# Performance work log

Measured on AMD Instinct MI355X. Metric: run time of the kernel, lower is better.

Reference implementation:

```python
import jax, jax.numpy as jnp
import numpy as np

N = 100000      # num graph nodes
E = 1600000     # num edges (avg degree 16)
IN = 128        # in_channels
H = 128         # hidden_channels
B = 4096        # query batch
CTX = 20        # context set length (indices[:, 3:])


def setup_inputs() -> dict:
    key = jax.random.key(0)
    ks = jax.random.split(key, 16)
    inp = {
        "indices": jax.random.randint(ks[0], (B, 3 + CTX), 0, N, dtype=jnp.int64),
        "src": jax.random.randint(ks[1], (E,), 0, N, dtype=jnp.int32),
        "dst": jax.random.randint(ks[2], (E,), 0, N, dtype=jnp.int32),
        "w": jax.random.uniform(ks[3], (E,), dtype=jnp.float32),
        # learned params
        "ndata": jax.random.normal(ks[4], (N, IN), dtype=jnp.float32),
        "W1": jax.random.normal(ks[5], (H, IN), dtype=jnp.float32) * (1.0 / np.sqrt(IN)),
        "b1": jnp.zeros((H,), jnp.float32),
        "W2": jax.random.normal(ks[6], (H, H), dtype=jnp.float32) * (1.0 / np.sqrt(H)),
        "b2": jnp.zeros((H,), jnp.float32),
        "eps": jnp.zeros((2,), jnp.float32),  # learn_eps, one per GINConv
        "Wc1": jax.random.normal(ks[7], (H, 3 * H), dtype=jnp.float32) * (1.0 / np.sqrt(3 * H)),
        "bc1": jnp.zeros((H,), jnp.float32),
        "Wc2": jax.random.normal(ks[8], (H // 2, H), dtype=jnp.float32) * (1.0 / np.sqrt(H)),
        "bc2": jnp.zeros((H // 2,), jnp.float32),
        "Wc3": jax.random.normal(ks[9], (1, H // 2), dtype=jnp.float32) * (1.0 / np.sqrt(H // 2)),
        "bc3": jnp.zeros((1,), jnp.float32),
    }
    return inp


def _gin_conv(x, src, dst, w, deg, eps, W, b):
    # DGL GINConv(mean, learn_eps): h = lin((1+eps)*x + mean_{in-edges}(w_e * x_src))
    msg = w[:, None] * x[src]                                   # [E, D]
    agg = jax.ops.segment_sum(msg, dst, num_segments=N) / deg   # [N, D]
    return ((1.0 + eps) * x + agg) @ W.T + b


def reference(indices, src, dst, w, ndata, W1, b1, W2, b2, eps,
              Wc1, bc1, Wc2, bc2, Wc3, bc3):
    deg = jax.ops.segment_sum(jnp.ones((E,), ndata.dtype), dst, num_segments=N)
    deg = jnp.maximum(deg, 1.0)[:, None]

    x = ndata
    x = jax.nn.relu(_gin_conv(x, src, dst, w, deg, eps[0], W1, b1))  # dropout inactive (eval)
    x = _gin_conv(x, src, dst, w, deg, eps[1], W2, b2)               # last layer: no relu
    x = x.at[0].set(0.0)                                             # x[0] = zeros

    ing1 = x[indices[:, 0]]   # [B, H]
    ing2 = x[indices[:, 1]]   # [B, H]

    # embed_context: mean over nonzero-index context members
    ctx_idx = indices[:, 3:]                                   # [B, CTX]
    ctx_sum = x[ctx_idx].sum(axis=1)                           # [B, H]
    norm = jnp.maximum((ctx_idx > 0).sum(axis=1), 1).astype(x.dtype)[:, None]
    ctx = ctx_sum / norm

    y = jnp.concatenate([ing1, ing2, ctx], axis=1)             # [B, 3H]
    y = jax.nn.relu(y @ Wc1.T + bc1)
    y = jax.nn.relu(y @ Wc2.T + bc2)
    y = y @ Wc3.T + bc3                                        # [B, 1]
    return y
```

## Files before the change

### kernel.cpp

```cpp
#include <hip/hip_runtime.h>


#define CONV_NPB 32

__global__ void init_kernel(const float* __restrict__ W1, const float* __restrict__ W2,
                            const float* __restrict__ Wc1, const float* __restrict__ Wc2,
                            float* __restrict__ Wt1, float* __restrict__ Wt2,
                            float* __restrict__ Wc1t, float* __restrict__ Wc2t,
                            int* __restrict__ cnt, int n) {
  int i = blockIdx.x * blockDim.x + threadIdx.x;
  if (i < n) cnt[i] = 0;
  if (i < 16384) {
    int f = i >> 7, k = i & 127;
    Wt1[k * 128 + f] = W1[i];
  } else if (i < 32768) {
    int j = i - 16384; int f = j >> 7, k = j & 127;
    Wt2[k * 128 + f] = W2[j];
  } else if (i < 81920) {
    int j = i - 32768; int f = j / 384, k = j % 384;
    Wc1t[k * 128 + f] = Wc1[j];
  } else if (i < 90112) {
    int j = i - 81920; int f = j >> 7, k = j & 127;
    Wc2t[k * 64 + f] = Wc2[j];
  }
}

__global__ void hist_kernel(const int* __restrict__ dst, int* __restrict__ cnt,
                            int* __restrict__ rank, int E) {
  int e = blockIdx.x * blockDim.x + threadIdx.x;
  if (e < E) rank[e] = atomicAdd(&cnt[dst[e]], 1);
}

__global__ void scan1_kernel(const int* __restrict__ cnt, int* __restrict__ prow,
                             int* __restrict__ bsum, int n) {
  __shared__ int smem[256];
  const int t = threadIdx.x;
  const int base = blockIdx.x * 2048 + t * 8;
  int v[8];
  int s = 0;
#pragma unroll
  for (int j = 0; j < 8; ++j) {
    int idx = base + j;
    v[j] = (idx < n) ? ((cnt[idx] + 7) & ~7) : 0;
    s += v[j];
  }
  smem[t] = s;
  __syncthreads();
  for (int off = 1; off < 256; off <<= 1) {
    int add = (t >= off) ? smem[t - off] : 0;
    __syncthreads();
    smem[t] += add;
    __syncthreads();
  }
  int run = smem[t] - s;
  if (t == 255) bsum[blockIdx.x] = smem[255];
#pragma unroll
  for (int j = 0; j < 8; ++j) {
    int idx = base + j;
    if (idx < n) prow[idx] = run;
    run += v[j];
  }
}

__global__ void scan2_kernel(int* __restrict__ bsum, int nb) {
  const int t = threadIdx.x;
  if (nb <= 64) {
    const int orig = (t < nb) ? bsum[t] : 0;
    int v = orig;
#pragma unroll
    for (int off = 1; off < 64; off <<= 1) {
      int u = __shfl_up(v, off);
      if (t >= off) v += u;
    }
    if (t == nb - 1) bsum[nb] = v;
    if (t < nb) bsum[t] = v - orig;
  } else if (t == 0) {
    int run = 0;
    for (int i = 0; i < nb; ++i) { int v = bsum[i]; bsum[i] = run; run += v; }
    bsum[nb] = run;
  }
}

__global__ void scatter_kernel(const int* __restrict__ src, const int* __restrict__ dst,
                               const float* __restrict__ w, const int* __restrict__ prow,
                               const int* __restrict__ bsum,
                               const int* __restrict__ rank, int2* __restrict__ epack, int E) {
  int e = blockIdx.x * blockDim.x + threadIdx.x;
  if (e < E) {
    const int d = dst[e];
    const int pos = prow[d] + bsum[d >> 11] + rank[e];
    epack[pos] = make_int2(src[e], __float_as_int(w[e]));
  }
}

__launch_bounds__(256, 6)
__global__ void conv_kernel(const float* __restrict__ xin, float* __restrict__ xout,
                            const int* __restrict__ prow, const int* __restrict__ bsum,
                            const int* __restrict__ cnt,
                            const int2* __restrict__ epack,
                            const float* __restrict__ Wt,
                            const float* __restrict__ bias, const float* __restrict__ eps,
                            int epsidx, int dorelu, int zerorow0, int n, int nchunk) {
  __shared__ float xm[CONV_NPB * 128];
  __shared__ int rp_s[CONV_NPB + 1];
  const int t = threadIdx.x;
  const int nb = blockIdx.x * CONV_NPB;
  const float epsv = 1.0f + eps[epsidx];

#pragma unroll
  for (int i = 0; i < 4; ++i)
    *(float4*)&xm[(t + i * 256) * 4] = make_float4(0.f, 0.f, 0.f, 0.f);
  if (t <= CONV_NPB) {
    const int node = nb + t;
    rp_s[t] = (node >= n) ? bsum[nchunk] : (prow[node] + bsum[node >> 11]);
  }
  __syncthreads();

  {
    const int L = t >> 5;
    const int lane = t & 31;
    const int f0 = lane * 4;
    const int e0 = rp_s[0], eT = rp_s[CONV_NPB];
    const int nbat = (eT - e0) >> 3;
    const int chunk = (((nbat + 7) >> 3)) << 3;
    const int jb = e0 + L * chunk;
    const int je = min(jb + chunk, eT);
    if (jb < je) {
      const int4* ep4 = (const int4*)epack;
      int r = 0;
      while (rp_s[r + 1] <= jb) ++r;
      float4 acc = make_float4(0.f, 0.f, 0.f, 0.f);
      for (int j = jb; j < je; j += 8) {
        if (rp_s[r + 1] <= j) {
          float* bp = &xm[r * 128 + lane];
          atomicAdd(bp + 0,  acc.x);
          atomicAdd(bp + 32, acc.y);
          atomicAdd(bp + 64, acc.z);
          atomicAdd(bp + 96, acc.w);
          acc = make_float4(0.f, 0.f, 0.f, 0.f);
          do { ++r; } while (rp_s[r + 1] <= j);
        }
        const int h = j >> 1;
        const int4 q0 = ep4[h + 0];
        const int4 q1 = ep4[h + 1];
        const int4 q2 = ep4[h + 2];
        const int4 q3 = ep4[h + 3];
        const float4 a0 = *(const float4*)&xin[(size_t)q0.x * 128 + f0];
        const float4 a1 = *(const float4*)&xin[(size_t)q0.z * 128 + f0];
        const float4 a2 = *(const float4*)&xin[(size_t)q1.x * 128 + f0];
        const float4 a3 = *(const float4*)&xin[(size_t)q1.z * 128 + f0];
        const float4 a4 = *(const float4*)&xin[(size_t)q2.x * 128 + f0];
        const float4 a5 = *(const float4*)&xin[(size_t)q2.z * 128 + f0];
        const float4 a6 = *(const float4*)&xin[(size_t)q3.x * 128 + f0];
        const float4 a7 = *(const float4*)&xin[(size_t)q3.z * 128 + f0];
        const float w0 = __int_as_float(q0.y), w1 = __int_as_float(q0.w);
        const float w2 = __int_as_float(q1.y), w3 = __int_as_float(q1.w);
        const float w4 = __int_as_float(q2.y), w5 = __int_as_float(q2.w);
        const float w6 = __int_as_float(q3.y), w7 = __int_as_float(q3.w);
        acc.x += w0 * a0.x + w1 * a1.x + w2 * a2.x + w3 * a3.x
               + w4 * a4.x + w5 * a5.x + w6 * a6.x + w7 * a7.x;
        acc.y += w0 * a0.y + w1 * a1.y + w2 * a2.y + w3 * a3.y
               + w4 * a4.y + w5 * a5.y + w6 * a6.y + w7 * a7.y;
        acc.z += w0 * a0.z + w1 * a1.z + w2 * a2.z + w3 * a3.z
               + w4 * a4.z + w5 * a5.z + w6 * a6.z + w7 * a7.z;
        acc.w += w0 * a0.w + w1 * a1.w + w2 * a2.w + w3 * a3.w
               + w4 * a4.w + w5 * a5.w + w6 * a6.w + w7 * a7.w;
      }
      float* bp = &xm[r * 128 + lane];
      atomicAdd(bp + 0,  acc.x);
      atomicAdd(bp + 32, acc.y);
      atomicAdd(bp + 64, acc.z);
      atomicAdd(bp + 96, acc.w);
    }
  }
  __syncthreads();

  {
    float4 m[4];
#pragma unroll
    for (int q = 0; q < 4; ++q) {
      const int task = t + q * 256;
      const int r = task >> 5;
      const int fg = task & 31;
      m[q].x = xm[r * 128 + fg];
      m[q].y = xm[r * 128 + 32 + fg];
      m[q].z = xm[r * 128 + 64 + fg];
      m[q].w = xm[r * 128 + 96 + fg];
    }
    __syncthreads();
#pragma unroll
    for (int q = 0; q < 4; ++q) {
      const int task = t + q * 256;
      const int r = task >> 5;
      const int fg = task & 31;
      const int f0 = fg * 4;
      const int node = nb + r;
      float4 v = make_float4(0.f, 0.f, 0.f, 0.f);
      if (node < n) {
        const int d = cnt[node];
        const float rdeg = 1.0f / (float)(d > 1 ? d : 1);
        const float4 xv = *(const float4*)&xin[(size_t)node * 128 + f0];
        v.x = epsv * xv.x + m[q].x * rdeg;
        v.y = epsv * xv.y + m[q].y * rdeg;
        v.z = epsv * xv.z + m[q].z * rdeg;
        v.w = epsv * xv.w + m[q].w * rdeg;
      }
      *(float4*)&xm[r * 128 + f0] = v;
    }
  }
  __syncthreads();

  {
    const int fg = t & 31;
    const int rg = t >> 5;
    const int f0 = fg * 4;
    const int r0 = rg * 4;
    float4 acc[4];
#pragma unroll
    for (int r = 0; r < 4; ++r) acc[r] = make_float4(0.f, 0.f, 0.f, 0.f);
    for (int k = 0; k < 128; k += 4) {
      const float4 w0 = *(const float4*)&Wt[(k + 0) * 128 + f0];
      const float4 w1 = *(const float4*)&Wt[(k + 1) * 128 + f0];
      const float4 w2 = *(const float4*)&Wt[(k + 2) * 128 + f0];
      const float4 w3 = *(const float4*)&Wt[(k + 3) * 128 + f0];
#pragma unroll
      for (int r = 0; r < 4; ++r) {
        const float4 xv = *(const float4*)&xm[(r0 + r) * 128 + k];
        acc[r].x += xv.x * w0.x + xv.y * w1.x + xv.z * w2.x + xv.w * w3.x;
        acc[r].y += xv.x * w0.y + xv.y * w1.y + xv.z * w2.y + xv.w * w3.y;
        acc[r].z += xv.x * w0.z + xv.y * w1.z + xv.z * w2.z + xv.w * w3.z;
        acc[r].w += xv.x * w0.w + xv.y * w1.w + xv.z * w2.w + xv.w * w3.w;
      }
    }
    const float4 bv = *(const float4*)&bias[f0];
#pragma unroll
    for (int r = 0; r < 4; ++r) {
      const int node = nb + r0 + r;
      if (node < n) {
        float4 v;
        v.x = acc[r].x + bv.x;
        v.y = acc[r].y + bv.y;
        v.z = acc[r].z + bv.z;
        v.w = acc[r].w + bv.w;
        if (dorelu) {
          v.x = fmaxf(v.x, 0.f); v.y = fmaxf(v.y, 0.f);
          v.z = fmaxf(v.z, 0.f); v.w = fmaxf(v.w, 0.f);
        }
        if (zerorow0 && node == 0) { v.x = 0.f; v.y = 0.f; v.z = 0.f; v.w = 0.f; }
        *(float4*)&xout[(size_t)node * 128 + f0] = v;
      }
    }
  }
}

__launch_bounds__(256, 4)
__global__ void final_kernel(const float* __restrict__ x2, const int* __restrict__ indices,
                             const float* __restrict__ Wc1t, const float* __restrict__ bc1,
                             const float* __restrict__ Wc2t, const float* __restrict__ bc2,
                             const float* __restrict__ Wc3, const float* __restrict__ bc3,
                             float* __restrict__ out) {
  __shared__ float ysm[16 * 384];
  __shared__ float h1s[16 * 128];
  __shared__ float h2s[16 * 64];
  __shared__ float ccs[16];
  const int t = threadIdx.x;
  const int b0 = blockIdx.x * 16;

#pragma unroll
  for (int q = 0; q < 8; ++q) {
    const int s = t + q * 256;
    ysm[(s >> 7) * 384 + 256 + (s & 127)] = 0.f;
  }
  if (t < 16) {
    const int* ind = indices + (size_t)(b0 + t) * 23;
    int cc = 0;
#pragma unroll
    for (int j = 0; j < 20; ++j) cc += (ind[3 + j] > 0) ? 1 : 0;
    ccs[t] = 1.0f / (float)(cc > 0 ? cc : 1);
  }
  __syncthreads();

  {
    const int f = t & 127;
    const int half = t >> 7;
#pragma unroll 1
    for (int e = 0; e < 16; ++e) {
      const int* ind = indices + (size_t)(b0 + e) * 23;
      const int ing = ind[half];
      ysm[e * 384 + half * 128 + f] = x2[(size_t)ing * 128 + f];
      float cs = 0.f;
#pragma unroll
      for (int j = 0; j < 10; ++j) {
        const int cj = ind[3 + half * 10 + j];
        cs += x2[(size_t)cj * 128 + f];
      }
      atomicAdd(&ysm[e * 384 + 256 + f], cs);
    }
  }
  __syncthreads();
#pragma unroll
  for (int q = 0; q < 8; ++q) {
    const int s = t + q * 256;
    const int e = s >> 7;
    ysm[e * 384 + 256 + (s & 127)] *= ccs[e];
  }
  __syncthreads();

  {
    const int f1 = t & 127;
    const int eh = t >> 7;
    float acc[8];
    const float b = bc1[f1];
#pragma unroll
    for (int i = 0; i < 8; ++i) acc[i] = b;
    for (int k = 0; k < 384; k += 4) {
      const float wv0 = Wc1t[(k + 0) * 128 + f1];
      const float wv1 = Wc1t[(k + 1) * 128 + f1];
      const float wv2 = Wc1t[(k + 2) * 128 + f1];
      const float wv3 = Wc1t[(k + 3) * 128 + f1];
#pragma unroll
      for (int i = 0; i < 8; ++i) {
        const float4 yv = *(const float4*)&ysm[(eh * 8 + i) * 384 + k];
        acc[i] += yv.x * wv0 + yv.y * wv1 + yv.z * wv2 + yv.w * wv3;
      }
    }
#pragma unroll
    for (int i = 0; i < 8; ++i)
      h1s[(eh * 8 + i) * 128 + f1] = fmaxf(acc[i], 0.f);
  }
  __syncthreads();

  {
    const int f2 = t & 63;
    const int eg = t >> 6;
    float acc[4];
    const float b = bc2[f2];
#pragma unroll
    for (int i = 0; i < 4; ++i) acc[i] = b;
    for (int k = 0; k < 128; k += 4) {
      const float wv0 = Wc2t[(k + 0) * 64 + f2];
      const float wv1 = Wc2t[(k + 1) * 64 + f2];
      const float wv2 = Wc2t[(k + 2) * 64 + f2];
      const float wv3 = Wc2t[(k + 3) * 64 + f2];
#pragma unroll
      for (int i = 0; i < 4; ++i) {
        const float4 hv = *(const float4*)&h1s[(eg * 4 + i) * 128 + k];
        acc[i] += hv.x * wv0 + hv.y * wv1 + hv.z * wv2 + hv.w * wv3;
      }
    }
#pragma unroll
    for (int i = 0; i < 4; ++i)
      h2s[(eg * 4 + i) * 64 + f2] = fmaxf(acc[i], 0.f);
  }
  __syncthreads();

  {
    const int e = t >> 4;
    const int l = t & 15;
    float p = 0.f;
#pragma unroll
    for (int k = 0; k < 4; ++k)
      p += h2s[e * 64 + l + k * 16] * Wc3[l + k * 16];
#pragma unroll
    for (int o = 8; o > 0; o >>= 1) p += __shfl_down(p, o, 16);
    if (l == 0) out[b0 + e] = p + bc3[0];
  }
}

extern "C" void kernel_launch(void* const* d_in, const int* in_sizes, int n_in,
                              void* d_out, int out_size, void* d_ws, size_t ws_size,
                              hipStream_t stream) {
  const int* indices = (const int*)d_in[0];
  const int* src = (const int*)d_in[1];
  const int* dst = (const int*)d_in[2];
  const float* w = (const float*)d_in[3];
  const float* ndata = (const float*)d_in[4];
  const float* W1 = (const float*)d_in[5];
  const float* b1 = (const float*)d_in[6];
  const float* W2 = (const float*)d_in[7];
  const float* b2 = (const float*)d_in[8];
  const float* eps = (const float*)d_in[9];
  const float* Wc1 = (const float*)d_in[10];
  const float* bc1 = (const float*)d_in[11];
  const float* Wc2 = (const float*)d_in[12];
  const float* bc2 = (const float*)d_in[13];
  const float* Wc3 = (const float*)d_in[14];
  const float* bc3 = (const float*)d_in[15];
  float* out = (float*)d_out;

  const int E = in_sizes[1];
  const int N = in_sizes[4] / 128;
  const int B = in_sizes[0] / 23;

  char* ws = (char*)d_ws;
  size_t off = 0;
  auto alloc = [&](size_t bytes) -> char* {
    char* p = ws + off;
    off = (off + bytes + 255) & ~(size_t)255;
    return p;
  };
  const size_t Epad = (size_t)E + 8 * (size_t)N;
  int* cnt = (int*)alloc((size_t)N * 4);
  int* prow = (int*)alloc((size_t)(N + 1) * 4);
  int* rank = (int*)alloc((size_t)E * 4);
  int* bsum = (int*)alloc(256 * 4);
  int2* epack = (int2*)alloc(Epad * 8);
  float* x1 = (float*)alloc((size_t)N * 128 * 4);
  float* x2 = (float*)alloc((size_t)N * 128 * 4);
  float* Wt1 = (float*)alloc(16384 * 4);
  float* Wt2 = (float*)alloc(16384 * 4);
  float* Wc1t = (float*)alloc(49152 * 4);
  float* Wc2t = (float*)alloc(8192 * 4);

  hipMemsetAsync(epack, 0, Epad * 8, stream);

  const int ninit = (N > 90112) ? N : 90112;
  init_kernel<<<(ninit + 255) / 256, 256, 0, stream>>>(W1, W2, Wc1, Wc2, Wt1, Wt2, Wc1t, Wc2t, cnt, N);
  hist_kernel<<<(E + 255) / 256, 256, 0, stream>>>(dst, cnt, rank, E);
  const int nchunk = (N + 2047) / 2048;
  scan1_kernel<<<nchunk, 256, 0, stream>>>(cnt, prow, bsum, N);
  scan2_kernel<<<1, 64, 0, stream>>>(bsum, nchunk);
  scatter_kernel<<<(E + 255) / 256, 256, 0, stream>>>(src, dst, w, prow, bsum, rank, epack, E);

  const int nconv = (N + CONV_NPB - 1) / CONV_NPB;
  conv_kernel<<<nconv, 256, 0, stream>>>(ndata, x1, prow, bsum, cnt, epack, Wt1, b1, eps, 0, 1, 0, N, nchunk);
  conv_kernel<<<nconv, 256, 0, stream>>>(x1, x2, prow, bsum, cnt, epack, Wt2, b2, eps, 1, 0, 1, N, nchunk);

  final_kernel<<<B / 16, 256, 0, stream>>>(x2, indices, Wc1t, bc1, Wc2t, bc2, Wc3, bc3, out);
}
```

Before: 601.4 us.

## Vectorize edge preprocessing and restructure final MLP with fewer queries per block

The histogram and scatter kernels now handle two edges per thread with int2/float2 loads, cutting thread count and load instructions. The final kernel processes 8 queries per block instead of 16, which doubles the block count for better occupancy. It also stages indices in shared memory and gathers x2 rows with float4 loads, summing all 20 context rows in registers instead of using shared-memory atomics. The cost is less reuse of the MLP weights per block, since Wc1/Wc2 are re-read by twice as many blocks.

```diff
diff --git a/kernel.cpp b/kernel.cpp
--- a/kernel.cpp
+++ b/kernel.cpp
@@ -2,6 +2,7 @@
 
 
 #define CONV_NPB 32
+#define FIN_EPB 8
 
 __global__ void init_kernel(const float* __restrict__ W1, const float* __restrict__ W2,
                             const float* __restrict__ Wc1, const float* __restrict__ Wc2,
@@ -27,8 +28,15 @@
 
 __global__ void hist_kernel(const int* __restrict__ dst, int* __restrict__ cnt,
                             int* __restrict__ rank, int E) {
-  int e = blockIdx.x * blockDim.x + threadIdx.x;
-  if (e < E) rank[e] = atomicAdd(&cnt[dst[e]], 1);
+  int e = (blockIdx.x * blockDim.x + threadIdx.x) * 2;
+  if (e + 1 < E) {
+    const int2 d = *(const int2*)&dst[e];
+    const int r0 = atomicAdd(&cnt[d.x], 1);
+    const int r1 = atomicAdd(&cnt[d.y], 1);
+    *(int2*)&rank[e] = make_int2(r0, r1);
+  } else if (e < E) {
+    rank[e] = atomicAdd(&cnt[dst[e]], 1);
+  }
 }
 
 __global__ void scan1_kernel(const int* __restrict__ cnt, int* __restrict__ prow,
@@ -85,8 +93,17 @@
                                const float* __restrict__ w, const int* __restrict__ prow,
                                const int* __restrict__ bsum,
                                const int* __restrict__ rank, int2* __restrict__ epack, int E) {
-  int e = blockIdx.x * blockDim.x + threadIdx.x;
-  if (e < E) {
+  int e = (blockIdx.x * blockDim.x + threadIdx.x) * 2;
+  if (e + 1 < E) {
+    const int2 d = *(const int2*)&dst[e];
+    const int2 s = *(const int2*)&src[e];
+    const float2 wv = *(const float2*)&w[e];
+    const int2 r = *(const int2*)&rank[e];
+    const int p0 = prow[d.x] + bsum[d.x >> 11] + r.x;
+    const int p1 = prow[d.y] + bsum[d.y >> 11] + r.y;
+    epack[p0] = make_int2(s.x, __float_as_int(wv.x));
+    epack[p1] = make_int2(s.y, __float_as_int(wv.y));
+  } else if (e < E) {
     const int d = dst[e];
     const int pos = prow[d] + bsum[d >> 11] + rank[e];
     epack[pos] = make_int2(src[e], __float_as_int(w[e]));
@@ -259,110 +276,104 @@
                              const float* __restrict__ Wc2t, const float* __restrict__ bc2,
                              const float* __restrict__ Wc3, const float* __restrict__ bc3,
                              float* __restrict__ out) {
-  __shared__ float ysm[16 * 384];
-  __shared__ float h1s[16 * 128];
-  __shared__ float h2s[16 * 64];
-  __shared__ float ccs[16];
+  __shared__ float ysm[FIN_EPB * 384];
+  __shared__ float h1s[FIN_EPB * 128];
+  __shared__ float h2s[FIN_EPB * 64];
+  __shared__ int ind_s[FIN_EPB * 23];
+  __shared__ float ccs[FIN_EPB];
   const int t = threadIdx.x;
-  const int b0 = blockIdx.x * 16;
-
-#pragma unroll
-  for (int q = 0; q < 8; ++q) {
-    const int s = t + q * 256;
-    ysm[(s >> 7) * 384 + 256 + (s & 127)] = 0.f;
-  }
-  if (t < 16) {
-    const int* ind = indices + (size_t)(b0 + t) * 23;
+  const int b0 = blockIdx.x * FIN_EPB;
+
+  if (t < FIN_EPB * 23) ind_s[t] = indices[(size_t)b0 * 23 + t];
+  __syncthreads();
+  if (t < FIN_EPB) {
     int cc = 0;
 #pragma unroll
-    for (int j = 0; j < 20; ++j) cc += (ind[3 + j] > 0) ? 1 : 0;
+    for (int j = 0; j < 20; ++j) cc += (ind_s[t * 23 + 3 + j] > 0) ? 1 : 0;
     ccs[t] = 1.0f / (float)(cc > 0 ? cc : 1);
   }
   __syncthreads();
 
   {
-    const int f = t & 127;
-    const int half = t >> 7;
-#pragma unroll 1
-    for (int e = 0; e < 16; ++e) {
-      const int* ind = indices + (size_t)(b0 + e) * 23;
-      const int ing = ind[half];
-      ysm[e * 384 + half * 128 + f] = x2[(size_t)ing * 128 + f];
-      float cs = 0.f;
-#pragma unroll
-      for (int j = 0; j < 10; ++j) {
-        const int cj = ind[3 + half * 10 + j];
-        cs += x2[(size_t)cj * 128 + f];
-      }
-      atomicAdd(&ysm[e * 384 + 256 + f], cs);
-    }
-  }
-  __syncthreads();
-#pragma unroll
-  for (int q = 0; q < 8; ++q) {
-    const int s = t + q * 256;
-    const int e = s >> 7;
-    ysm[e * 384 + 256 + (s & 127)] *= ccs[e];
+#pragma unroll
+    for (int q = 0; q < 2; ++q) {
+      const int s = t + q * 256;
+      const int e = s >> 6;
+      const int half = (s >> 5) & 1;
+      const int fg = s & 31;
+      const int idx = ind_s[e * 23 + half];
+      *(float4*)&ysm[e * 384 + half * 128 + fg * 4] =
+          *(const float4*)&x2[(size_t)idx * 128 + fg * 4];
+    }
+    const int e = t >> 5;
+    const int fg = t & 31;
+    float4 acc = make_float4(0.f, 0.f, 0.f, 0.f);
+#pragma unroll
+    for (int j = 0; j < 20; ++j) {
+      const int cj = ind_s[e * 23 + 3 + j];
+      const float4 a = *(const float4*)&x2[(size_t)cj * 128 + fg * 4];
+      acc.x += a.x; acc.y += a.y; acc.z += a.z; acc.w += a.w;
+    }
+    const float sc = ccs[e];
+    acc.x *= sc; acc.y *= sc; acc.z *= sc; acc.w *= sc;
+    *(float4*)&ysm[e * 384 + 256 + fg * 4] = acc;
   }
   __syncthreads();
 
   {
     const int f1 = t & 127;
     const int eh = t >> 7;
-    float acc[8];
+    float acc[4];
     const float b = bc1[f1];
 #pragma unroll
-    for (int i = 0; i < 8; ++i) acc[i] = b;
+    for (int i = 0; i < 4; ++i) acc[i] = b;
     for (int k = 0; k < 384; k += 4) {
       const float wv0 = Wc1t[(k + 0) * 128 + f1];
       const float wv1 = Wc1t[(k + 1) * 128 + f1];
       const float wv2 = Wc1t[(k + 2) * 128 + f1];
       const float wv3 = Wc1t[(k + 3) * 128 + f1];
 #pragma unroll
-      for (int i = 0; i < 8; ++i) {
-        const float4 yv = *(const float4*)&ysm[(eh * 8 + i) * 384 + k];
+      for (int i = 0; i < 4; ++i) {
+        const float4 yv = *(const float4*)&ysm[(eh * 4 + i) * 384 + k];
         acc[i] += yv.x * wv0 + yv.y * wv1 + yv.z * wv2 + yv.w * wv3;
       }
     }
 #pragma unroll
-    for (int i = 0; i < 8; ++i)
-      h1s[(eh * 8 + i) * 128 + f1] = fmaxf(acc[i], 0.f);
+    for (int i = 0; i < 4; ++i)
+      h1s[(eh * 4 + i) * 128 + f1] = fmaxf(acc[i], 0.f);
   }
   __syncthreads();
 
   {
     const int f2 = t & 63;
     const int eg = t >> 6;
-    float acc[4];
+    float acc[2];
     const float b = bc2[f2];
 #pragma unroll
-    for (int i = 0; i < 4; ++i) acc[i] = b;
+    for (int i = 0; i < 2; ++i) acc[i] = b;
     for (int k = 0; k < 128; k += 4) {
       const float wv0 = Wc2t[(k + 0) * 64 + f2];
       const float wv1 = Wc2t[(k + 1) * 64 + f2];
       const float wv2 = Wc2t[(k + 2) * 64 + f2];
       const float wv3 = Wc2t[(k + 3) * 64 + f2];
 #pragma unroll
-      for (int i = 0; i < 4; ++i) {
-        const float4 hv = *(const float4*)&h1s[(eg * 4 + i) * 128 + k];
+      for (int i = 0; i < 2; ++i) {
+        const float4 hv = *(const float4*)&h1s[(eg * 2 + i) * 128 + k];
         acc[i] += hv.x * wv0 + hv.y * wv1 + hv.z * wv2 + hv.w * wv3;
       }
     }
 #pragma unroll
-    for (int i = 0; i < 4; ++i)
-      h2s[(eg * 4 + i) * 64 + f2] = fmaxf(acc[i], 0.f);
-  }
-  __syncthreads();
-
-  {
-    const int e = t >> 4;
-    const int l = t & 15;
-    float p = 0.f;
-#pragma unroll
-    for (int k = 0; k < 4; ++k)
-      p += h2s[e * 64 + l + k * 16] * Wc3[l + k * 16];
-#pragma unroll
-    for (int o = 8; o > 0; o >>= 1) p += __shfl_down(p, o, 16);
+    for (int i = 0; i < 2; ++i)
+      h2s[(eg * 2 + i) * 64 + f2] = fmaxf(acc[i], 0.f);
+  }
+  __syncthreads();
+
+  {
+    const int e = t >> 5;
+    const int l = t & 31;
+    float p = h2s[e * 64 + l] * Wc3[l] + h2s[e * 64 + l + 32] * Wc3[l + 32];
+#pragma unroll
+    for (int o = 16; o > 0; o >>= 1) p += __shfl_down(p, o, 32);
     if (l == 0) out[b0 + e] = p + bc3[0];
   }
 }
@@ -416,15 +427,16 @@
 
   const int ninit = (N > 90112) ? N : 90112;
   init_kernel<<<(ninit + 255) / 256, 256, 0, stream>>>(W1, W2, Wc1, Wc2, Wt1, Wt2, Wc1t, Wc2t, cnt, N);
-  hist_kernel<<<(E + 255) / 256, 256, 0, stream>>>(dst, cnt, rank, E);
+  const int Eh = (E + 1) / 2;
+  hist_kernel<<<(Eh + 255) / 256, 256, 0, stream>>>(dst, cnt, rank, E);
   const int nchunk = (N + 2047) / 2048;
   scan1_kernel<<<nchunk, 256, 0, stream>>>(cnt, prow, bsum, N);
   scan2_kernel<<<1, 64, 0, stream>>>(bsum, nchunk);
-  scatter_kernel<<<(E + 255) / 256, 256, 0, stream>>>(src, dst, w, prow, bsum, rank, epack, E);
+  scatter_kernel<<<(Eh + 255) / 256, 256, 0, stream>>>(src, dst, w, prow, bsum, rank, epack, E);
 
   const int nconv = (N + CONV_NPB - 1) / CONV_NPB;
   conv_kernel<<<nconv, 256, 0, stream>>>(ndata, x1, prow, bsum, cnt, epack, Wt1, b1, eps, 0, 1, 0, N, nchunk);
   conv_kernel<<<nconv, 256, 0, stream>>>(x1, x2, prow, bsum, cnt, epack, Wt2, b2, eps, 1, 0, 1, N, nchunk);
 
-  final_kernel<<<B / 16, 256, 0, stream>>>(x2, indices, Wc1t, bc1, Wc2t, bc2, Wc3, bc3, out);
-}
+  final_kernel<<<B / FIN_EPB, 256, 0, stream>>>(x2, indices, Wc1t, bc1, Wc2t, bc2, Wc3, bc3, out);
+}
```

Result: no change. 597.6 us (-0.6%).
